# Optimization experiments

Measured on AMD Instinct MI355X. Metric: run time of the kernel, lower is better.

Reference implementation:

```python
import jax, jax.numpy as jnp
import numpy as np
from jax import lax

B, T, C, H, HOR = 64, 2048, 64, 256, 96
BETA, THR = 0.9, 1.0


def setup_inputs() -> dict:
    key = jax.random.key(0)
    ks = jax.random.split(key, 10)
    s = lambda *sh: 1.0 / np.sqrt(sh[-1])
    return {
        "x": jax.random.normal(ks[0], (B, T, C), jnp.float32),
        "snn_w": jax.random.uniform(ks[1], (H, C), jnp.float32, -s(C), s(C)),
        "snn_b": jax.random.uniform(ks[2], (H,), jnp.float32, -s(C), s(C)),
        "gru_wih": jax.random.uniform(ks[3], (3 * H, C + H), jnp.float32, -s(H), s(H)),
        "gru_whh": jax.random.uniform(ks[4], (3 * H, H), jnp.float32, -s(H), s(H)),
        "gru_bih": jax.random.uniform(ks[5], (3 * H,), jnp.float32, -s(H), s(H)),
        "gru_bhh": jax.random.uniform(ks[6], (3 * H,), jnp.float32, -s(H), s(H)),
        "head_w": jax.random.uniform(ks[7], (HOR, H), jnp.float32, -s(H), s(H)),
        "head_b": jax.random.uniform(ks[8], (HOR,), jnp.float32, -s(H), s(H)),
    }


@jax.custom_vjp
def spike(x):
    return (x > 0).astype(x.dtype)

def _spike_fwd(x):
    return spike(x), x

def _spike_bwd(x, g):
    # snntorch ATan surrogate, alpha=2: grad = 1 / (1 + (pi*x)^2)
    return (g / (1.0 + (jnp.pi * x) ** 2),)

spike.defvjp(_spike_fwd, _spike_bwd)


def reference(x, snn_w, snn_b, gru_wih, gru_whh, gru_bih, gru_bhh, head_w, head_b):
    # Batched SNN input current across all timesteps: [B,T,H]
    cur = jnp.einsum("btc,hc->bth", x, snn_w) + snn_b

    def lif_step(mem, i_t):
        # reset computed from previous mem, detached (snntorch mem_reset)
        reset = lax.stop_gradient((mem > THR).astype(mem.dtype))
        mem_new = BETA * mem + i_t - reset * THR
        spk = spike(mem_new - THR)
        return mem_new, spk

    mem0 = jnp.zeros((B, H), x.dtype)
    _, spks = lax.scan(lif_step, mem0, cur.transpose(1, 0, 2))  # [T,B,H]

    h_comb = jnp.concatenate([x, spks.transpose(1, 0, 2)], axis=-1)  # [B,T,C+H]

    # GRU: precompute input gates for all timesteps
    gx = jnp.einsum("btc,gc->btg", h_comb, gru_wih) + gru_bih  # [B,T,3H]

    def gru_step(h, gx_t):
        gh = h @ gru_whh.T + gru_bhh
        xr, xz, xn = jnp.split(gx_t, 3, axis=-1)
        hr, hz, hn = jnp.split(gh, 3, axis=-1)
        r = jax.nn.sigmoid(xr + hr)
        z = jax.nn.sigmoid(xz + hz)
        n = jnp.tanh(xn + r * hn)
        h_new = (1.0 - z) * n + z * h
        return h_new, None

    h0 = jnp.zeros((B, H), x.dtype)
    hT, _ = lax.scan(gru_step, h0, gx.transpose(1, 0, 2))

    return hT @ head_w.T + head_b  # [B, HOR]
```

## Files before the change

kernel.cpp:

```cpp
#include <hip/hip_runtime.h>
#include <cstdint>
#include <cstddef>

#define B_   64
#define T_   2048
#define C_   64
#define H_   256
#define G3_  768
#define HOR_ 96

typedef _Float16 h2 __attribute__((ext_vector_type(2)));
typedef _Float16 h8 __attribute__((ext_vector_type(8)));
typedef _Float16 f16x8 __attribute__((ext_vector_type(8)));
typedef float f32x4 __attribute__((ext_vector_type(4)));

#define K1_TT 128
__global__ __launch_bounds__(256) void k_cur(const float* __restrict__ x,
                                             const float* __restrict__ w,
                                             const float* __restrict__ bias,
                                             float* __restrict__ cur,
                                             int* __restrict__ flags) {
  __shared__ float xs[K1_TT * C_];
  const int b = blockIdx.x;
  const int t0 = blockIdx.y * K1_TT;
  const int tid = threadIdx.x;

  if (b == 0 && blockIdx.y == 0) {
#pragma unroll
    for (int i = 0; i < 4; i++) flags[tid + i * 256] = 0;
  }

  const float4* xsrc = (const float4*)(x + ((size_t)b * T_ + t0) * C_);
  float4* xdst = (float4*)xs;
#pragma unroll
  for (int i = 0; i < (K1_TT * C_ / 4) / 256; i++)
    xdst[tid + i * 256] = xsrc[tid + i * 256];

  float wr[C_];
  const float4* wp = (const float4*)(w + (size_t)tid * C_);
#pragma unroll
  for (int q = 0; q < C_ / 4; q++) {
    float4 v = wp[q];
    wr[4 * q + 0] = v.x; wr[4 * q + 1] = v.y;
    wr[4 * q + 2] = v.z; wr[4 * q + 3] = v.w;
  }
  const float bb = bias[tid];
  __syncthreads();

  for (int t = 0; t < K1_TT; t++) {
    const float4* xrow = (const float4*)(xs + t * C_);
    float a0 = 0.f, a1 = 0.f;
#pragma unroll
    for (int q = 0; q < C_ / 4; q += 2) {
      float4 v0 = xrow[q];
      float4 v1 = xrow[q + 1];
      a0 += wr[4 * q + 0] * v0.x + wr[4 * q + 1] * v0.y +
            wr[4 * q + 2] * v0.z + wr[4 * q + 3] * v0.w;
      a1 += wr[4 * q + 4] * v1.x + wr[4 * q + 5] * v1.y +
            wr[4 * q + 6] * v1.z + wr[4 * q + 7] * v1.w;
    }
    cur[((size_t)b * T_ + t0 + t) * H_ + tid] = a0 + a1 + bb;
  }
}

__global__ __launch_bounds__(64) void k_lif(const float* __restrict__ cur,
                                            unsigned char* __restrict__ spk) {
  const int b = blockIdx.x >> 2;
  const int h = ((blockIdx.x & 3) << 6) + threadIdx.x;
  const float* cp = cur + (size_t)b * T_ * H_ + h;
  unsigned char* sp = spk + (size_t)b * T_ * H_ + h;
  float mem = 0.f;
#pragma unroll 32
  for (int t = 0; t < T_; t++) {
    float c = cp[(size_t)t * H_];
    float reset = (mem > 1.0f) ? 1.0f : 0.0f;
    mem = 0.9f * mem + c - reset;
    sp[(size_t)t * H_] = (mem > 1.0f) ? (unsigned char)1 : (unsigned char)0;
  }
}

#define GM 128
#define GN 128
#define AKP 40
#define CTP 136
#define DQ_ (0.0625f / (127.0f * 127.0f))
__global__ __launch_bounds__(512, 2) void k_fused(
    const float* __restrict__ x, const unsigned char* __restrict__ spk,
    const float* __restrict__ wih, const float* __restrict__ bih,
    _Float16* __restrict__ gx, const float* __restrict__ whh,
    const float* __restrict__ bhh, const float* __restrict__ head_w,
    const float* __restrict__ head_b, float* __restrict__ out,
    int* __restrict__ flags) {
  alignas(16) __shared__ _Float16 Ah[GM * AKP];
  alignas(16) __shared__ _Float16 Bh[GN * AKP];
  alignas(16) __shared__ _Float16 Ct[GM * CTP];
  alignas(16) __shared__ int hq[2][64];
  __shared__ float hbuf32[H_];

  const int tid = threadIdx.x;
  const int lane = tid & 63;

  if (blockIdx.x >= 64) {
    const int pidx = blockIdx.x - 64;
    const int bb = pidx / 3;
    const int pp = pidx - bb * 3;
    const int wave = tid >> 6;
    const int ln = lane & 15;
    const int qd = lane >> 4;
    const int wm = (wave & 1) * 64;
    const int wn = (wave >> 1) * 32;

    for (int mt = 0; mt < 16; mt++) {
      const int m0 = bb * 2048 + mt * 128;
      for (int nh = 0; nh < 2; nh++) {
        const int n0 = pp * 256 + nh * 128;
        f32x4 acc[4][2] = {};
        for (int kc = 0; kc < 10; kc++) {
          const int k0 = kc * 32;
          if (k0 < 64) {
#pragma unroll
            for (int i = 0; i < 2; i++) {
              int idx = tid + i * 512;
              int r = idx >> 3;
              int c4 = (idx & 7) * 4;
              float4 v = *(const float4*)(x + (size_t)(m0 + r) * C_ + k0 + c4);
              h2 lo, hi;
              lo.x = (_Float16)v.x; lo.y = (_Float16)v.y;
              hi.x = (_Float16)v.z; hi.y = (_Float16)v.w;
              h2* d = (h2*)&Ah[r * AKP + c4];
              d[0] = lo; d[1] = hi;
            }
          } else {
#pragma unroll
            for (int i = 0; i < 2; i++) {
              int idx = tid + i * 512;
              int r = idx >> 3;
              int c4 = (idx & 7) * 4;
              uchar4 u = *(const uchar4*)(spk + (size_t)(m0 + r) * H_ + (k0 - 64) + c4);
              h2 lo, hi;
              lo.x = (_Float16)(int)u.x; lo.y = (_Float16)(int)u.y;
              hi.x = (_Float16)(int)u.z; hi.y = (_Float16)(int)u.w;
              h2* d = (h2*)&Ah[r * AKP + c4];
              d[0] = lo; d[1] = hi;
            }
          }
#pragma unroll
          for (int i = 0; i < 2; i++) {
            int idx = tid + i * 512;
            int r = idx >> 3;
            int c4 = (idx & 7) * 4;
            float4 v = *(const float4*)(wih + (size_t)(n0 + r) * 320 + k0 + c4);
            h2 lo, hi;
            lo.x = (_Float16)v.x; lo.y = (_Float16)v.y;
            hi.x = (_Float16)v.z; hi.y = (_Float16)v.w;
            h2* d = (h2*)&Bh[r * AKP + c4];
            d[0] = lo; d[1] = hi;
          }
          __syncthreads();
          {
            f16x8 a[4], bbf[2];
#pragma unroll
            for (int mtl = 0; mtl < 4; mtl++)
              a[mtl] = *(const f16x8*)&Ah[(wm + mtl * 16 + ln) * AKP + qd * 8];
#pragma unroll
            for (int nt = 0; nt < 2; nt++)
              bbf[nt] = *(const f16x8*)&Bh[(wn + nt * 16 + ln) * AKP + qd * 8];
#pragma unroll
            for (int mtl = 0; mtl < 4; mtl++)
#pragma unroll
              for (int nt = 0; nt < 2; nt++)
                acc[mtl][nt] = __builtin_amdgcn_mfma_f32_16x16x32_f16(
                    a[mtl], bbf[nt], acc[mtl][nt], 0, 0, 0);
          }
          __syncthreads();
        }
        {
          float bias[2];
#pragma unroll
          for (int nt = 0; nt < 2; nt++) bias[nt] = bih[n0 + wn + nt * 16 + ln];
#pragma unroll
          for (int mtl = 0; mtl < 4; mtl++)
#pragma unroll
            for (int nt = 0; nt < 2; nt++) {
              int n = wn + nt * 16 + ln;
#pragma unroll
              for (int r = 0; r < 4; r++) {
                int m = wm + mtl * 16 + qd * 4 + r;
                Ct[m * CTP + n] = (_Float16)(acc[mtl][nt][r] + bias[nt]);
              }
            }
        }
        __syncthreads();
#pragma unroll
        for (int i = 0; i < 4; i++) {
          int idx = tid + i * 512;
          int r = idx >> 4;
          int c = (idx & 15) * 8;
          *(h8*)(gx + (size_t)(m0 + r) * G3_ + n0 + c) = *(const h8*)&Ct[r * CTP + c];
        }
        __syncthreads();
      }
      if (tid == 0)
        __hip_atomic_fetch_add(&flags[bb * 16 + mt], 1, __ATOMIC_RELEASE,
                               __HIP_MEMORY_SCOPE_AGENT);
    }
    return;
  }

  const int b = blockIdx.x;
  const int j = tid >> 1;
  const int half = tid & 1;

  int wr[32], wz[32], wn2[32];
  {
    const float qs = 2032.0f;
    const float4* p0 = (const float4*)(whh + (size_t)j * H_ + half * 128);
    const float4* p1 = (const float4*)(whh + (size_t)(H_ + j) * H_ + half * 128);
    const float4* p2 = (const float4*)(whh + (size_t)(2 * H_ + j) * H_ + half * 128);
#pragma unroll
    for (int q = 0; q < 32; q++) {
      float4 a = p0[q];
      wr[q] = ((int)rintf(a.x * qs) & 255) | (((int)rintf(a.y * qs) & 255) << 8) |
              (((int)rintf(a.z * qs) & 255) << 16) | (((int)rintf(a.w * qs) & 255) << 24);
      float4 c = p1[q];
      wz[q] = ((int)rintf(c.x * qs) & 255) | (((int)rintf(c.y * qs) & 255) << 8) |
              (((int)rintf(c.z * qs) & 255) << 16) | (((int)rintf(c.w * qs) & 255) << 24);
      float4 d = p2[q];
      wn2[q] = ((int)rintf(d.x * qs) & 255) | (((int)rintf(d.y * qs) & 255) << 8) |
               (((int)rintf(d.z * qs) & 255) << 16) | (((int)rintf(d.w * qs) & 255) << 24);
    }
  }
  const float br_ = bhh[j], bz_ = bhh[H_ + j], bn_ = bhh[2 * H_ + j];

  if (tid < 128) ((int*)hq)[tid] = 0;
  float hj = 0.f;
  __syncthreads();

  const _Float16* gxb = gx + (size_t)b * T_ * G3_;
  int p = 0;
  for (int mt = 0; mt < 16; mt++) {
    if (tid == 0) {
      while (__hip_atomic_load(&flags[b * 16 + mt], __ATOMIC_ACQUIRE,
                               __HIP_MEMORY_SCOPE_AGENT) < 3)
        __builtin_amdgcn_s_sleep(8);
    }
    __syncthreads();

    const _Float16* gc = gxb + (size_t)mt * 128 * G3_;
    _Float16 pr = gc[j], pz = gc[H_ + j], pn = gc[2 * H_ + j];

    for (int tt = 0; tt < 128; tt++) {
      float xr = (float)pr, xz = (float)pz, xn = (float)pn;
      if (tt < 127) {
        const _Float16* g = gc + (size_t)(tt + 1) * G3_;
        pr = g[j]; pz = g[H_ + j]; pn = g[2 * H_ + j];
      }

      const int* hb = hq[p] + (half << 5);
      int ar0 = 0, ar1 = 0, az0 = 0, az1 = 0, an0 = 0, an1 = 0;
#pragma unroll
      for (int c = 0; c < 8; c++) {
        int4 hv = ((const int4*)hb)[c];
#pragma unroll
        for (int i = 0; i < 4; i++) {
          int h4 = (i == 0) ? hv.x : (i == 1) ? hv.y : (i == 2) ? hv.z : hv.w;
          int wi = c * 4 + i;
          if (wi & 1) {
            ar1 = __builtin_amdgcn_sdot4(wr[wi], h4, ar1, false);
            az1 = __builtin_amdgcn_sdot4(wz[wi], h4, az1, false);
            an1 = __builtin_amdgcn_sdot4(wn2[wi], h4, an1, false);
          } else {
            ar0 = __builtin_amdgcn_sdot4(wr[wi], h4, ar0, false);
            az0 = __builtin_amdgcn_sdot4(wz[wi], h4, az0, false);
            an0 = __builtin_amdgcn_sdot4(wn2[wi], h4, an0, false);
          }
        }
      }
      int ar = ar0 + ar1; ar += __shfl_xor(ar, 1);
      int az = az0 + az1; az += __shfl_xor(az, 1);
      int an = an0 + an1; an += __shfl_xor(an, 1);

      float r = 1.f / (1.f + __expf(-(xr + (float)ar * DQ_ + br_)));
      float z = 1.f / (1.f + __expf(-(xz + (float)az * DQ_ + bz_)));
      float pre = xn + r * ((float)an * DQ_ + bn_);
      float e = __expf(2.f * pre);
      float n = 1.f - 2.f / (e + 1.f);
      hj = (1.f - z) * n + z * hj;

      if (!half) ((char*)hq[p ^ 1])[j] = (char)(int)rintf(hj * 127.0f);
      p ^= 1;
      __syncthreads();
    }
  }

  if (!half) hbuf32[j] = hj;
  __syncthreads();

  if (tid < HOR_) {
    const float4* hw = (const float4*)(head_w + (size_t)tid * H_);
    const float4* hv4 = (const float4*)hbuf32;
    float acc = head_b[tid];
#pragma unroll
    for (int q = 0; q < H_ / 4; q++) {
      float4 w4 = hw[q];
      float4 v4 = hv4[q];
      acc += w4.x * v4.x + w4.y * v4.y + w4.z * v4.z + w4.w * v4.w;
    }
    out[(size_t)b * HOR_ + tid] = acc;
  }
}

extern "C" void kernel_launch(void* const* d_in, const int* in_sizes, int n_in,
                              void* d_out, int out_size, void* d_ws, size_t ws_size,
                              hipStream_t stream) {
  const float* x      = (const float*)d_in[0];
  const float* snn_w  = (const float*)d_in[1];
  const float* snn_b  = (const float*)d_in[2];
  const float* wih    = (const float*)d_in[3];
  const float* whh    = (const float*)d_in[4];
  const float* bih    = (const float*)d_in[5];
  const float* bhh    = (const float*)d_in[6];
  const float* head_w = (const float*)d_in[7];
  const float* head_b = (const float*)d_in[8];
  float* out = (float*)d_out;

  char* ws = (char*)d_ws;
  _Float16* gx = (_Float16*)ws;
  float* cur = (float*)ws;
  unsigned char* spk = (unsigned char*)(ws + (size_t)201326592);
  int* flags = (int*)(ws + (size_t)234881024);

  k_cur<<<dim3(B_, T_ / K1_TT), 256, 0, stream>>>(x, snn_w, snn_b, cur, flags);
  k_lif<<<dim3(256), 64, 0, stream>>>(cur, spk);
  k_fused<<<dim3(256), 512, 0, stream>>>(x, spk, wih, bih, gx, whh, bhh,
                                         head_w, head_b, out, flags);
}
```

Measured before the change: 2.043 ms.

## Batch 16 sequences per GRU block using int8 MFMA for recurrent matvec

New measurement: 6.763 ms. +231.1%, slower.

```diff
diff --git a/kernel.cpp b/kernel.cpp
--- a/kernel.cpp
+++ b/kernel.cpp
@@ -10,9 +10,11 @@
 #define HOR_ 96
 
 typedef _Float16 h2 __attribute__((ext_vector_type(2)));
+typedef _Float16 h4v __attribute__((ext_vector_type(4)));
 typedef _Float16 h8 __attribute__((ext_vector_type(8)));
 typedef _Float16 f16x8 __attribute__((ext_vector_type(8)));
 typedef float f32x4 __attribute__((ext_vector_type(4)));
+typedef int i32x4 __attribute__((ext_vector_type(4)));
 
 #define K1_TT 128
 __global__ __launch_bounds__(256) void k_cur(const float* __restrict__ x,
@@ -83,8 +85,10 @@
 #define GN 128
 #define AKP 40
 #define CTP 136
+#define HQP 288
 #define DQ_ (0.0625f / (127.0f * 127.0f))
-__global__ __launch_bounds__(512, 2) void k_fused(
+__global__ __attribute__((amdgpu_flat_work_group_size(512, 512),
+                          amdgpu_waves_per_eu(2))) void k_fused(
     const float* __restrict__ x, const unsigned char* __restrict__ spk,
     const float* __restrict__ wih, const float* __restrict__ bih,
     _Float16* __restrict__ gx, const float* __restrict__ whh,
@@ -94,14 +98,14 @@
   alignas(16) __shared__ _Float16 Ah[GM * AKP];
   alignas(16) __shared__ _Float16 Bh[GN * AKP];
   alignas(16) __shared__ _Float16 Ct[GM * CTP];
-  alignas(16) __shared__ int hq[2][64];
-  __shared__ float hbuf32[H_];
+  alignas(16) __shared__ unsigned char hlds[2][16][HQP];
+  alignas(16) __shared__ float hb32[16][H_];
 
   const int tid = threadIdx.x;
   const int lane = tid & 63;
 
-  if (blockIdx.x >= 64) {
-    const int pidx = blockIdx.x - 64;
+  if (blockIdx.x >= 4) {
+    const int pidx = blockIdx.x - 4;
     const int bb = pidx / 3;
     const int pp = pidx - bb * 3;
     const int wave = tid >> 6;
@@ -207,106 +211,130 @@
     return;
   }
 
-  const int b = blockIdx.x;
-  const int j = tid >> 1;
-  const int half = tid & 1;
-
-  int wr[32], wz[32], wn2[32];
+  const int b0 = blockIdx.x << 4;
+  const int w = tid >> 6;
+  const int lb = lane & 15;
+  const int lk = lane >> 4;
+
+  i32x4 wf[6][4];
   {
     const float qs = 2032.0f;
-    const float4* p0 = (const float4*)(whh + (size_t)j * H_ + half * 128);
-    const float4* p1 = (const float4*)(whh + (size_t)(H_ + j) * H_ + half * 128);
-    const float4* p2 = (const float4*)(whh + (size_t)(2 * H_ + j) * H_ + half * 128);
-#pragma unroll
-    for (int q = 0; q < 32; q++) {
-      float4 a = p0[q];
-      wr[q] = ((int)rintf(a.x * qs) & 255) | (((int)rintf(a.y * qs) & 255) << 8) |
-              (((int)rintf(a.z * qs) & 255) << 16) | (((int)rintf(a.w * qs) & 255) << 24);
-      float4 c = p1[q];
-      wz[q] = ((int)rintf(c.x * qs) & 255) | (((int)rintf(c.y * qs) & 255) << 8) |
-              (((int)rintf(c.z * qs) & 255) << 16) | (((int)rintf(c.w * qs) & 255) << 24);
-      float4 d = p2[q];
-      wn2[q] = ((int)rintf(d.x * qs) & 255) | (((int)rintf(d.y * qs) & 255) << 8) |
-               (((int)rintf(d.z * qs) & 255) << 16) | (((int)rintf(d.w * qs) & 255) << 24);
-    }
-  }
-  const float br_ = bhh[j], bz_ = bhh[H_ + j], bn_ = bhh[2 * H_ + j];
-
-  if (tid < 128) ((int*)hq)[tid] = 0;
-  float hj = 0.f;
+#pragma unroll
+    for (int g = 0; g < 3; g++)
+#pragma unroll
+      for (int s = 0; s < 2; s++) {
+        const float* row = whh + (size_t)(g * 256 + w * 32 + s * 16 + lb) * H_;
+#pragma unroll
+        for (int c = 0; c < 4; c++) {
+          const int kb = c * 64 + lk * 16;
+          i32x4 v;
+#pragma unroll
+          for (int d = 0; d < 4; d++) {
+            float4 f = *(const float4*)(row + kb + d * 4);
+            v[d] = ((int)rintf(f.x * qs) & 255) | (((int)rintf(f.y * qs) & 255) << 8) |
+                   (((int)rintf(f.z * qs) & 255) << 16) | (((int)rintf(f.w * qs) & 255) << 24);
+          }
+          wf[g * 2 + s][c] = v;
+        }
+      }
+  }
+  float bR[8], bZ[8], bN[8];
+#pragma unroll
+  for (int s = 0; s < 2; s++)
+#pragma unroll
+    for (int r = 0; r < 4; r++) {
+      const int jj = w * 32 + s * 16 + lk * 4 + r;
+      bR[s * 4 + r] = bhh[jj];
+      bZ[s * 4 + r] = bhh[H_ + jj];
+      bN[s * 4 + r] = bhh[2 * H_ + jj];
+    }
+  float ho[8] = {0.f, 0.f, 0.f, 0.f, 0.f, 0.f, 0.f, 0.f};
+
+  for (int i = tid; i < (int)(2 * 16 * HQP / 4); i += 512) ((int*)hlds)[i] = 0;
   __syncthreads();
 
-  const _Float16* gxb = gx + (size_t)b * T_ * G3_;
+  const _Float16* gxT = gx + (size_t)(b0 + lb) * T_ * G3_ + w * 32 + lk * 4;
   int p = 0;
   for (int mt = 0; mt < 16; mt++) {
-    if (tid == 0) {
-      while (__hip_atomic_load(&flags[b * 16 + mt], __ATOMIC_ACQUIRE,
+    if (tid < 16) {
+      while (__hip_atomic_load(&flags[(b0 + tid) * 16 + mt], __ATOMIC_ACQUIRE,
                                __HIP_MEMORY_SCOPE_AGENT) < 3)
         __builtin_amdgcn_s_sleep(8);
     }
     __syncthreads();
 
-    const _Float16* gc = gxb + (size_t)mt * 128 * G3_;
-    _Float16 pr = gc[j], pz = gc[H_ + j], pn = gc[2 * H_ + j];
-
     for (int tt = 0; tt < 128; tt++) {
-      float xr = (float)pr, xz = (float)pz, xn = (float)pn;
-      if (tt < 127) {
-        const _Float16* g = gc + (size_t)(tt + 1) * G3_;
-        pr = g[j]; pz = g[H_ + j]; pn = g[2 * H_ + j];
+      const _Float16* gp = gxT + (size_t)(mt * 128 + tt) * G3_;
+      h4v gv[6];
+#pragma unroll
+      for (int g = 0; g < 3; g++)
+#pragma unroll
+        for (int s = 0; s < 2; s++)
+          gv[g * 2 + s] = *(const h4v*)(gp + g * 256 + s * 16);
+
+      i32x4 hf[4];
+#pragma unroll
+      for (int c = 0; c < 4; c++)
+        hf[c] = *(const i32x4*)&hlds[p][lb][c * 64 + lk * 16];
+
+      i32x4 acc[6];
+#pragma unroll
+      for (int idx = 0; idx < 6; idx++) {
+        i32x4 a = {0, 0, 0, 0};
+#pragma unroll
+        for (int c = 0; c < 4; c++)
+          a = __builtin_amdgcn_mfma_i32_16x16x64_i8(wf[idx][c], hf[c], a, 0, 0, 0);
+        acc[idx] = a;
       }
 
-      const int* hb = hq[p] + (half << 5);
-      int ar0 = 0, ar1 = 0, az0 = 0, az1 = 0, an0 = 0, an1 = 0;
-#pragma unroll
-      for (int c = 0; c < 8; c++) {
-        int4 hv = ((const int4*)hb)[c];
-#pragma unroll
-        for (int i = 0; i < 4; i++) {
-          int h4 = (i == 0) ? hv.x : (i == 1) ? hv.y : (i == 2) ? hv.z : hv.w;
-          int wi = c * 4 + i;
-          if (wi & 1) {
-            ar1 = __builtin_amdgcn_sdot4(wr[wi], h4, ar1, false);
-            az1 = __builtin_amdgcn_sdot4(wz[wi], h4, az1, false);
-            an1 = __builtin_amdgcn_sdot4(wn2[wi], h4, an1, false);
-          } else {
-            ar0 = __builtin_amdgcn_sdot4(wr[wi], h4, ar0, false);
-            az0 = __builtin_amdgcn_sdot4(wz[wi], h4, az0, false);
-            an0 = __builtin_amdgcn_sdot4(wn2[wi], h4, an0, false);
-          }
-        }
+#pragma unroll
+      for (int s = 0; s < 2; s++) {
+        int packed = 0;
+#pragma unroll
+        for (int r = 0; r < 4; r++) {
+          const float xr = (float)gv[s][r];
+          const float xz = (float)gv[2 + s][r];
+          const float xn = (float)gv[4 + s][r];
+          const float ar = (float)acc[s][r] * DQ_ + bR[s * 4 + r];
+          const float az = (float)acc[2 + s][r] * DQ_ + bZ[s * 4 + r];
+          const float an = (float)acc[4 + s][r] * DQ_ + bN[s * 4 + r];
+          const float rr = 1.f / (1.f + __expf(-(xr + ar)));
+          const float zz = 1.f / (1.f + __expf(-(xz + az)));
+          const float pre = xn + rr * an;
+          const float e = __expf(2.f * pre);
+          const float nn = 1.f - 2.f / (e + 1.f);
+          const float h = (1.f - zz) * nn + zz * ho[s * 4 + r];
+          ho[s * 4 + r] = h;
+          packed |= ((int)rintf(h * 127.0f) & 255) << (8 * r);
+        }
+        *(int*)&hlds[p ^ 1][lb][w * 32 + s * 16 + lk * 4] = packed;
       }
-      int ar = ar0 + ar1; ar += __shfl_xor(ar, 1);
-      int az = az0 + az1; az += __shfl_xor(az, 1);
-      int an = an0 + an1; an += __shfl_xor(an, 1);
-
-      float r = 1.f / (1.f + __expf(-(xr + (float)ar * DQ_ + br_)));
-      float z = 1.f / (1.f + __expf(-(xz + (float)az * DQ_ + bz_)));
-      float pre = xn + r * ((float)an * DQ_ + bn_);
-      float e = __expf(2.f * pre);
-      float n = 1.f - 2.f / (e + 1.f);
-      hj = (1.f - z) * n + z * hj;
-
-      if (!half) ((char*)hq[p ^ 1])[j] = (char)(int)rintf(hj * 127.0f);
       p ^= 1;
       __syncthreads();
     }
   }
 
-  if (!half) hbuf32[j] = hj;
+#pragma unroll
+  for (int s = 0; s < 2; s++)
+#pragma unroll
+    for (int r = 0; r < 4; r++)
+      hb32[lb][w * 32 + s * 16 + lk * 4 + r] = ho[s * 4 + r];
   __syncthreads();
 
-  if (tid < HOR_) {
-    const float4* hw = (const float4*)(head_w + (size_t)tid * H_);
-    const float4* hv4 = (const float4*)hbuf32;
-    float acc = head_b[tid];
+#pragma unroll
+  for (int i = 0; i < 3; i++) {
+    const int o = tid + i * 512;
+    const int bb2 = o / 96, rr2 = o % 96;
+    const float4* hw = (const float4*)(head_w + (size_t)rr2 * H_);
+    const float4* hv = (const float4*)&hb32[bb2][0];
+    float acc2 = head_b[rr2];
 #pragma unroll
     for (int q = 0; q < H_ / 4; q++) {
       float4 w4 = hw[q];
-      float4 v4 = hv4[q];
-      acc += w4.x * v4.x + w4.y * v4.y + w4.z * v4.z + w4.w * v4.w;
-    }
-    out[(size_t)b * HOR_ + tid] = acc;
+      float4 v4 = hv[q];
+      acc2 += w4.x * v4.x + w4.y * v4.y + w4.z * v4.z + w4.w * v4.w;
+    }
+    out[(size_t)(b0 + bb2) * HOR_ + rr2] = acc2;
   }
 }
 
@@ -332,6 +360,6 @@
 
   k_cur<<<dim3(B_, T_ / K1_TT), 256, 0, stream>>>(x, snn_w, snn_b, cur, flags);
   k_lif<<<dim3(256), 64, 0, stream>>>(cur, spk);
-  k_fused<<<dim3(256), 512, 0, stream>>>(x, spk, wih, bih, gx, whh, bhh,
+  k_fused<<<dim3(196), 512, 0, stream>>>(x, spk, wih, bih, gx, whh, bhh,
                                          head_w, head_b, out, flags);
 }
```
